# Kernel optimization log

Hardware: AMD Instinct MI355X
Metric: run time of the kernel (lower is better)

The kernel has to match this reference:

```python
import jax, jax.numpy as jnp
import numpy as np

N_NODES = 100000
N_EDGES = 1600000
D_IN = 128
D_OUT = 128


def setup_inputs() -> dict:
    key = jax.random.key(0)
    k1, k2, k3, k4 = jax.random.split(key, 4)
    feat = jax.random.normal(k1, (N_NODES, D_IN), dtype=jnp.float32)
    # xavier_uniform on [D_IN, D_OUT]
    limit = float(np.sqrt(6.0 / (D_IN + D_OUT)))
    weight = jax.random.uniform(k2, (D_IN, D_OUT), minval=-limit, maxval=limit, dtype=jnp.float32)
    bias = jnp.zeros((D_OUT,), dtype=jnp.float32)
    src = jax.random.randint(k3, (N_EDGES,), 0, N_NODES, dtype=jnp.int32)
    dst = jax.random.randint(k4, (N_EDGES,), 0, N_NODES, dtype=jnp.int32)
    return {"feat": feat, "weight": weight, "bias": bias, "src": src, "dst": dst}


def reference(feat, weight, bias, src, dst):
    n = feat.shape[0]
    # in-degree of each node (number of incoming edges)
    deg = jax.ops.segment_sum(jnp.ones_like(dst, dtype=feat.dtype), dst, num_segments=n)
    norm = jnp.power(jnp.clip(deg, 1.0), -0.5)[:, None]  # [N, 1]
    # pre-normalize source features
    h = feat * norm
    # copy_src + sum aggregation: scatter-add messages from src to dst
    agg = jax.ops.segment_sum(h[src], dst, num_segments=n)  # [N, D_IN]
    # in_feats == out_feats -> matmul after aggregation (the else-branch)
    rst = jnp.matmul(agg, weight)
    rst = rst * norm + bias
    return rst
```

## Files before the change

### kernel.cpp

```cpp
#include <hip/hip_runtime.h>

#define D 128
#define BSHIFT 7
#define BNODES 128
#define BMASK 127
#define NB_MAX 1024
#define STRIDE 2944
#define BIN_CHUNK 4096

typedef unsigned int uint;
typedef __attribute__((ext_vector_type(8))) short bf16x8;
typedef __attribute__((ext_vector_type(4))) float f32x4;

__device__ inline uint bf16_rne(float x) {
    uint u = __float_as_uint(x);
    return (u + 0x7fffu + ((u >> 16) & 1u)) >> 16;
}
__device__ inline uint pack2(float lo, float hi) {
    return bf16_rne(lo) | (bf16_rne(hi) << 16);
}

__global__ void __launch_bounds__(256) bin_kernel(const int* __restrict__ src,
                                                  const int* __restrict__ dst,
                                                  int* __restrict__ bucket_cur,
                                                  uint* __restrict__ binned,
                                                  const float* __restrict__ W,
                                                  uint4* __restrict__ wpack,
                                                  int n_edges, int nchunks) {
    int t = threadIdx.x;
    if (blockIdx.x == (uint)nchunks) {
        for (int idx = t; idx < 2048; idx += 256) {
            int lane = idx & 63;
            int ks = (idx >> 6) & 3;
            int ct = idx >> 8;
            int col = ct * 16 + (lane & 15);
            int k0 = ks * 32 + (lane >> 4) * 8;
            uint4 u;
            u.x = pack2(W[(k0 + 0) * D + col], W[(k0 + 1) * D + col]);
            u.y = pack2(W[(k0 + 2) * D + col], W[(k0 + 3) * D + col]);
            u.z = pack2(W[(k0 + 4) * D + col], W[(k0 + 5) * D + col]);
            u.w = pack2(W[(k0 + 6) * D + col], W[(k0 + 7) * D + col]);
            wpack[idx] = u;
        }
        return;
    }

    __shared__ int h[NB_MAX];
    __shared__ int base[NB_MAX];
    long long e0 = (long long)blockIdx.x * BIN_CHUNK;
    for (int j = t; j < NB_MAX; j += 256) h[j] = 0;
    __syncthreads();

    int d[16], s[16];
#pragma unroll
    for (int k = 0; k < 16; ++k) {
        long long idx = e0 + k * 256 + t;
        if (idx < n_edges) {
            d[k] = dst[idx];
            s[k] = src[idx];
            atomicAdd(&h[d[k] >> BSHIFT], 1);
        } else {
            d[k] = -1;
        }
    }
    __syncthreads();
    for (int j = t; j < NB_MAX; j += 256) {
        int c = h[j];
        base[j] = c ? atomicAdd(&bucket_cur[j], c) : 0;
        h[j] = 0;
    }
    __syncthreads();
#pragma unroll
    for (int k = 0; k < 16; ++k) {
        if (d[k] >= 0) {
            int b = d[k] >> BSHIFT;
            int r = base[b] + atomicAdd(&h[b], 1);
            if (r < STRIDE)
                binned[(size_t)b * STRIDE + r] =
                    ((uint)s[k] << BSHIFT) | (uint)(d[k] & BMASK);
        }
    }
}

__global__ void __launch_bounds__(256) fill2_kernel(
        const int* __restrict__ bucket_cur, uint* __restrict__ csr,
        int* __restrict__ row_start, int* __restrict__ degp, int n_nodes) {
    __shared__ uint sbin[STRIDE];
    __shared__ int deg[BNODES];
    __shared__ int rs[BNODES];
    __shared__ int cur[BNODES];
    int b = blockIdx.x;
    int t = threadIdx.x;
    int cnt = bucket_cur[b];
    if (cnt > STRIDE) cnt = STRIDE;
    size_t gbase = (size_t)b * STRIDE;

    for (int k = t; k < cnt; k += 256) sbin[k] = csr[gbase + k];
    if (t < BNODES) deg[t] = 0;
    __syncthreads();
    for (int k = t; k < cnt; k += 256) atomicAdd(&deg[sbin[k] & BMASK], 1);
    __syncthreads();

    int v = 0;
    if (t < BNODES) {
        v = deg[t];
        rs[t] = v;
    }
    __syncthreads();
    for (int o = 1; o < BNODES; o <<= 1) {
        int a = (t < BNODES && t >= o) ? rs[t - o] : 0;
        __syncthreads();
        if (t < BNODES) rs[t] += a;
        __syncthreads();
    }
    if (t < BNODES) {
        int excl = rs[t] - v;
        rs[t] = excl;
        cur[t] = 0;
        int node = b * BNODES + t;
        if (node < n_nodes) {
            row_start[node] = (int)gbase + excl;
            degp[node] = v;
        }
    }
    __syncthreads();

    for (int k = t; k < cnt; k += 256) {
        uint p = sbin[k];
        int dl = p & BMASK;
        int r = atomicAdd(&cur[dl], 1);
        csr[gbase + rs[dl] + r] = p >> BSHIFT;
    }
}

#define GP_ROWS 64
#define GLDP 132
__global__ void __launch_bounds__(256) gemm_prep_kernel(
        const float* __restrict__ feat, const int* __restrict__ degp,
        const uint4* __restrict__ wpack, uint* __restrict__ g32, int n) {
    __shared__ float As[GP_ROWS][GLDP];
    int t = threadIdx.x;
    int lane = t & 63;
    int w = t >> 6;
    int r0 = blockIdx.x * GP_ROWS;

    for (int idx = t; idx < GP_ROWS * 32; idx += 256) {
        int row = idx >> 5;
        int p = idx & 31;
        int gr = r0 + row;
        if (gr >= n) gr = n - 1;
        float4 f = *(const float4*)(feat + (size_t)gr * D + p * 4);
        *(float4*)&As[row][p * 4] = f;
    }
    __syncthreads();

    int c = lane & 15;
    int g = lane >> 4;
    int rbase = w * 16;

    uint4 afr[4];
#pragma unroll
    for (int ks = 0; ks < 4; ++ks) {
        const float* ap = &As[rbase + c][ks * 32 + g * 8];
        float4 f0 = *(const float4*)ap;
        float4 f1 = *(const float4*)(ap + 4);
        afr[ks].x = pack2(f0.x, f0.y);
        afr[ks].y = pack2(f0.z, f0.w);
        afr[ks].z = pack2(f1.x, f1.y);
        afr[ks].w = pack2(f1.z, f1.w);
    }

    float nm[4];
#pragma unroll
    for (int r = 0; r < 4; ++r) {
        int gr = r0 + rbase + g * 4 + r;
        int rc = gr < n ? gr : n - 1;
        nm[r] = rsqrtf(fmaxf((float)degp[rc], 1.0f));
    }

#pragma unroll
    for (int ct = 0; ct < 8; ++ct) {
        f32x4 acc = {0.f, 0.f, 0.f, 0.f};
#pragma unroll
        for (int ks = 0; ks < 4; ++ks) {
            uint4 bu = wpack[(ct * 4 + ks) * 64 + lane];
            acc = __builtin_amdgcn_mfma_f32_16x16x32_bf16(
                *(bf16x8*)&afr[ks], *(bf16x8*)&bu, acc, 0, 0, 0);
        }
#pragma unroll
        for (int r = 0; r < 4; ++r)
            As[rbase + g * 4 + r][ct * 16 + c] = acc[r] * nm[r];
    }

    for (int idx = lane; idx < 16 * 64; idx += 64) {
        int row = idx >> 6;
        int j = idx & 63;
        int gr = r0 + rbase + row;
        if (gr < n) {
            uint vpk = pack2(As[rbase + row][2 * j], As[rbase + row][2 * j + 1]);
            g32[(size_t)gr * 64 + j] = vpk;
        }
    }
}

#define UNPACK_ADD(u)                              \
    acc[0] += __uint_as_float((u).x << 16);        \
    acc[1] += __uint_as_float((u).x & 0xffff0000u);\
    acc[2] += __uint_as_float((u).y << 16);        \
    acc[3] += __uint_as_float((u).y & 0xffff0000u);\
    acc[4] += __uint_as_float((u).z << 16);        \
    acc[5] += __uint_as_float((u).z & 0xffff0000u);\
    acc[6] += __uint_as_float((u).w << 16);        \
    acc[7] += __uint_as_float((u).w & 0xffff0000u);

__global__ void __launch_bounds__(256) gather_out_kernel(
        const uint4* __restrict__ g128, const uint* __restrict__ csr,
        const int* __restrict__ row_start, const int* __restrict__ degp,
        const float* __restrict__ bias, float* __restrict__ out, int n) {
    int lane = threadIdx.x & 63;
    int wid = threadIdx.x >> 6;
    int i = blockIdx.x * 4 + wid;
    if (i >= n) return;
    int g = lane >> 4;
    int c = lane & 15;
    float4 b_lo = *(const float4*)(bias + 8 * c);
    float4 b_hi = *(const float4*)(bias + 8 * c + 4);

    int beg = row_start[i];
    int dv = degp[i];
    int end = beg + dv;
    float acc[8];
#pragma unroll
    for (int j = 0; j < 8; ++j) acc[j] = 0.f;

    for (int base = beg; base < end; base += 64) {
        int nk = end - base;
        if (nk > 64) nk = 64;
        int epre = (base + lane < end) ? (int)csr[base + lane] : 0;
        int k = 0;
        int kfull = nk & ~7;
        for (; k < kfull; k += 8) {
            int s0 = __shfl(epre, k + g, 64);
            int s1 = __shfl(epre, k + 4 + g, 64);
            uint4 u0 = g128[(size_t)s0 * 16 + c];
            uint4 u1 = g128[(size_t)s1 * 16 + c];
            UNPACK_ADD(u0);
            UNPACK_ADD(u1);
        }
        if (k < nk) {
            int e0 = k + g;
            int e1 = k + 4 + g;
            int s0 = __shfl(epre, e0 & 63, 64);
            int s1 = __shfl(epre, e1 & 63, 64);
            uint4 z = {0u, 0u, 0u, 0u};
            uint4 u0 = (e0 < nk) ? g128[(size_t)s0 * 16 + c] : z;
            uint4 u1 = (e1 < nk) ? g128[(size_t)s1 * 16 + c] : z;
            UNPACK_ADD(u0);
            UNPACK_ADD(u1);
        }
    }

#pragma unroll
    for (int j = 0; j < 8; ++j) {
        acc[j] += __shfl_xor(acc[j], 16, 64);
        acc[j] += __shfl_xor(acc[j], 32, 64);
    }
    if (g == 0) {
        float nrm = rsqrtf(fmaxf((float)dv, 1.0f));
        float4 lo, hi;
        lo.x = acc[0] * nrm + b_lo.x;
        lo.y = acc[1] * nrm + b_lo.y;
        lo.z = acc[2] * nrm + b_lo.z;
        lo.w = acc[3] * nrm + b_lo.w;
        hi.x = acc[4] * nrm + b_hi.x;
        hi.y = acc[5] * nrm + b_hi.y;
        hi.z = acc[6] * nrm + b_hi.z;
        hi.w = acc[7] * nrm + b_hi.w;
        float* orow = out + (size_t)i * D + 8 * c;
        *(float4*)orow = lo;
        *(float4*)(orow + 4) = hi;
    }
}

extern "C" void kernel_launch(void* const* d_in, const int* in_sizes, int n_in,
                              void* d_out, int out_size, void* d_ws, size_t ws_size,
                              hipStream_t stream) {
    const float* feat   = (const float*)d_in[0];
    const float* weight = (const float*)d_in[1];
    const float* bias   = (const float*)d_in[2];
    const int*   src    = (const int*)d_in[3];
    const int*   dst    = (const int*)d_in[4];
    float* out = (float*)d_out;

    int n_nodes = in_sizes[0] / D;
    int n_edges = in_sizes[3];
    int nb = (n_nodes + BNODES - 1) >> BSHIFT;
    int nchunks = (n_edges + BIN_CHUNK - 1) / BIN_CHUNK;

    int*   degp       = (int*)d_ws;
    int*   row_start  = degp + n_nodes;
    int*   bucket_cur = row_start + n_nodes;
    uint*  csr        = (uint*)(bucket_cur + NB_MAX);
    uint*  g32        = csr + (size_t)nb * STRIDE;
    uint4* wpack      = (uint4*)(g32 + (size_t)n_nodes * 64);

    hipMemsetAsync(bucket_cur, 0, NB_MAX * sizeof(int), stream);

    bin_kernel<<<nchunks + 1, 256, 0, stream>>>(src, dst, bucket_cur, csr,
                                                weight, wpack, n_edges, nchunks);
    fill2_kernel<<<nb, 256, 0, stream>>>(bucket_cur, csr, row_start, degp,
                                         n_nodes);
    gemm_prep_kernel<<<(n_nodes + GP_ROWS - 1) / GP_ROWS, 256, 0, stream>>>(
        feat, degp, wpack, g32, n_nodes);
    gather_out_kernel<<<(n_nodes + 3) / 4, 256, 0, stream>>>(
        (const uint4*)g32, csr, row_start, degp, bias, out, n_nodes);
}
```

Measured before the change: 139.0 us.

## Overlap edge binning with feature GEMM by deferring source norm to gather

Removes the GEMM's dependency on degrees by applying the source-side norm in the gather, via a per-node norm array computed in fill. Because of that, the binning and feature-transform GEMM run as independent block ranges of one kernel. The memset and the weight packing move into a small init kernel. The gather now loads one extra norm per edge and does an extra multiply per element, in exchange for overlapping the two front-end stages.

```diff
diff --git a/kernel.cpp b/kernel.cpp
--- a/kernel.cpp
+++ b/kernel.cpp
@@ -7,6 +7,8 @@
 #define NB_MAX 1024
 #define STRIDE 2944
 #define BIN_CHUNK 4096
+#define GP_ROWS 64
+#define GLDP 132
 
 typedef unsigned int uint;
 typedef __attribute__((ext_vector_type(8))) short bf16x8;
@@ -20,15 +22,13 @@
     return bf16_rne(lo) | (bf16_rne(hi) << 16);
 }
 
-__global__ void __launch_bounds__(256) bin_kernel(const int* __restrict__ src,
-                                                  const int* __restrict__ dst,
-                                                  int* __restrict__ bucket_cur,
-                                                  uint* __restrict__ binned,
-                                                  const float* __restrict__ W,
-                                                  uint4* __restrict__ wpack,
-                                                  int n_edges, int nchunks) {
+__global__ void __launch_bounds__(256) init_kernel(int* __restrict__ bucket_cur,
+                                                   const float* __restrict__ W,
+                                                   uint4* __restrict__ wpack) {
     int t = threadIdx.x;
-    if (blockIdx.x == (uint)nchunks) {
+    if (blockIdx.x == 0) {
+        for (int j = t; j < NB_MAX; j += 256) bucket_cur[j] = 0;
+    } else {
         for (int idx = t; idx < 2048; idx += 256) {
             int lane = idx & 63;
             int ks = (idx >> 6) & 3;
@@ -42,49 +42,115 @@
             u.w = pack2(W[(k0 + 6) * D + col], W[(k0 + 7) * D + col]);
             wpack[idx] = u;
         }
+    }
+}
+
+__global__ void __launch_bounds__(256) mega_kernel(
+        const int* __restrict__ src, const int* __restrict__ dst,
+        int* __restrict__ bucket_cur, uint* __restrict__ binned,
+        const float* __restrict__ feat, const uint4* __restrict__ wpack,
+        uint* __restrict__ g32, int n_edges, int nchunks, int n) {
+    __shared__ float As[GP_ROWS][GLDP];
+    int t = threadIdx.x;
+
+    if (blockIdx.x < (uint)nchunks) {
+        int* h = (int*)&As[0][0];
+        int* base = h + NB_MAX;
+        long long e0 = (long long)blockIdx.x * BIN_CHUNK;
+        for (int j = t; j < NB_MAX; j += 256) h[j] = 0;
+        __syncthreads();
+
+        int d[16], s[16];
+#pragma unroll
+        for (int k = 0; k < 16; ++k) {
+            long long idx = e0 + k * 256 + t;
+            if (idx < n_edges) {
+                d[k] = dst[idx];
+                s[k] = src[idx];
+                atomicAdd(&h[d[k] >> BSHIFT], 1);
+            } else {
+                d[k] = -1;
+            }
+        }
+        __syncthreads();
+        for (int j = t; j < NB_MAX; j += 256) {
+            int c = h[j];
+            base[j] = c ? atomicAdd(&bucket_cur[j], c) : 0;
+            h[j] = 0;
+        }
+        __syncthreads();
+#pragma unroll
+        for (int k = 0; k < 16; ++k) {
+            if (d[k] >= 0) {
+                int b = d[k] >> BSHIFT;
+                int r = base[b] + atomicAdd(&h[b], 1);
+                if (r < STRIDE)
+                    binned[(size_t)b * STRIDE + r] =
+                        ((uint)s[k] << BSHIFT) | (uint)(d[k] & BMASK);
+            }
+        }
         return;
     }
 
-    __shared__ int h[NB_MAX];
-    __shared__ int base[NB_MAX];
-    long long e0 = (long long)blockIdx.x * BIN_CHUNK;
-    for (int j = t; j < NB_MAX; j += 256) h[j] = 0;
-    __syncthreads();
-
-    int d[16], s[16];
-#pragma unroll
-    for (int k = 0; k < 16; ++k) {
-        long long idx = e0 + k * 256 + t;
-        if (idx < n_edges) {
-            d[k] = dst[idx];
-            s[k] = src[idx];
-            atomicAdd(&h[d[k] >> BSHIFT], 1);
-        } else {
-            d[k] = -1;
-        }
-    }
-    __syncthreads();
-    for (int j = t; j < NB_MAX; j += 256) {
-        int c = h[j];
-        base[j] = c ? atomicAdd(&bucket_cur[j], c) : 0;
-        h[j] = 0;
-    }
-    __syncthreads();
-#pragma unroll
-    for (int k = 0; k < 16; ++k) {
-        if (d[k] >= 0) {
-            int b = d[k] >> BSHIFT;
-            int r = base[b] + atomicAdd(&h[b], 1);
-            if (r < STRIDE)
-                binned[(size_t)b * STRIDE + r] =
-                    ((uint)s[k] << BSHIFT) | (uint)(d[k] & BMASK);
+    int lane = t & 63;
+    int w = t >> 6;
+    int r0 = (blockIdx.x - nchunks) * GP_ROWS;
+
+    for (int idx = t; idx < GP_ROWS * 32; idx += 256) {
+        int row = idx >> 5;
+        int p = idx & 31;
+        int gr = r0 + row;
+        if (gr >= n) gr = n - 1;
+        float4 f = *(const float4*)(feat + (size_t)gr * D + p * 4);
+        *(float4*)&As[row][p * 4] = f;
+    }
+    __syncthreads();
+
+    int c = lane & 15;
+    int g = lane >> 4;
+    int rbase = w * 16;
+
+    uint4 afr[4];
+#pragma unroll
+    for (int ks = 0; ks < 4; ++ks) {
+        const float* ap = &As[rbase + c][ks * 32 + g * 8];
+        float4 f0 = *(const float4*)ap;
+        float4 f1 = *(const float4*)(ap + 4);
+        afr[ks].x = pack2(f0.x, f0.y);
+        afr[ks].y = pack2(f0.z, f0.w);
+        afr[ks].z = pack2(f1.x, f1.y);
+        afr[ks].w = pack2(f1.z, f1.w);
+    }
+
+#pragma unroll
+    for (int ct = 0; ct < 8; ++ct) {
+        f32x4 acc = {0.f, 0.f, 0.f, 0.f};
+#pragma unroll
+        for (int ks = 0; ks < 4; ++ks) {
+            uint4 bu = wpack[(ct * 4 + ks) * 64 + lane];
+            acc = __builtin_amdgcn_mfma_f32_16x16x32_bf16(
+                *(bf16x8*)&afr[ks], *(bf16x8*)&bu, acc, 0, 0, 0);
+        }
+#pragma unroll
+        for (int r = 0; r < 4; ++r)
+            As[rbase + g * 4 + r][ct * 16 + c] = acc[r];
+    }
+
+    for (int idx = lane; idx < 16 * 64; idx += 64) {
+        int row = idx >> 6;
+        int j = idx & 63;
+        int gr = r0 + rbase + row;
+        if (gr < n) {
+            uint vpk = pack2(As[rbase + row][2 * j], As[rbase + row][2 * j + 1]);
+            g32[(size_t)gr * 64 + j] = vpk;
         }
     }
 }
 
 __global__ void __launch_bounds__(256) fill2_kernel(
         const int* __restrict__ bucket_cur, uint* __restrict__ csr,
-        int* __restrict__ row_start, int* __restrict__ degp, int n_nodes) {
+        int* __restrict__ row_start, int* __restrict__ degp,
+        float* __restrict__ norm, int n_nodes) {
     __shared__ uint sbin[STRIDE];
     __shared__ int deg[BNODES];
     __shared__ int rs[BNODES];
@@ -121,6 +187,7 @@
         if (node < n_nodes) {
             row_start[node] = (int)gbase + excl;
             degp[node] = v;
+            norm[node] = rsqrtf(fmaxf((float)v, 1.0f));
         }
     }
     __syncthreads();
@@ -133,90 +200,21 @@
     }
 }
 
-#define GP_ROWS 64
-#define GLDP 132
-__global__ void __launch_bounds__(256) gemm_prep_kernel(
-        const float* __restrict__ feat, const int* __restrict__ degp,
-        const uint4* __restrict__ wpack, uint* __restrict__ g32, int n) {
-    __shared__ float As[GP_ROWS][GLDP];
-    int t = threadIdx.x;
-    int lane = t & 63;
-    int w = t >> 6;
-    int r0 = blockIdx.x * GP_ROWS;
-
-    for (int idx = t; idx < GP_ROWS * 32; idx += 256) {
-        int row = idx >> 5;
-        int p = idx & 31;
-        int gr = r0 + row;
-        if (gr >= n) gr = n - 1;
-        float4 f = *(const float4*)(feat + (size_t)gr * D + p * 4);
-        *(float4*)&As[row][p * 4] = f;
-    }
-    __syncthreads();
-
-    int c = lane & 15;
-    int g = lane >> 4;
-    int rbase = w * 16;
-
-    uint4 afr[4];
-#pragma unroll
-    for (int ks = 0; ks < 4; ++ks) {
-        const float* ap = &As[rbase + c][ks * 32 + g * 8];
-        float4 f0 = *(const float4*)ap;
-        float4 f1 = *(const float4*)(ap + 4);
-        afr[ks].x = pack2(f0.x, f0.y);
-        afr[ks].y = pack2(f0.z, f0.w);
-        afr[ks].z = pack2(f1.x, f1.y);
-        afr[ks].w = pack2(f1.z, f1.w);
-    }
-
-    float nm[4];
-#pragma unroll
-    for (int r = 0; r < 4; ++r) {
-        int gr = r0 + rbase + g * 4 + r;
-        int rc = gr < n ? gr : n - 1;
-        nm[r] = rsqrtf(fmaxf((float)degp[rc], 1.0f));
-    }
-
-#pragma unroll
-    for (int ct = 0; ct < 8; ++ct) {
-        f32x4 acc = {0.f, 0.f, 0.f, 0.f};
-#pragma unroll
-        for (int ks = 0; ks < 4; ++ks) {
-            uint4 bu = wpack[(ct * 4 + ks) * 64 + lane];
-            acc = __builtin_amdgcn_mfma_f32_16x16x32_bf16(
-                *(bf16x8*)&afr[ks], *(bf16x8*)&bu, acc, 0, 0, 0);
-        }
-#pragma unroll
-        for (int r = 0; r < 4; ++r)
-            As[rbase + g * 4 + r][ct * 16 + c] = acc[r] * nm[r];
-    }
-
-    for (int idx = lane; idx < 16 * 64; idx += 64) {
-        int row = idx >> 6;
-        int j = idx & 63;
-        int gr = r0 + rbase + row;
-        if (gr < n) {
-            uint vpk = pack2(As[rbase + row][2 * j], As[rbase + row][2 * j + 1]);
-            g32[(size_t)gr * 64 + j] = vpk;
-        }
-    }
-}
-
-#define UNPACK_ADD(u)                              \
-    acc[0] += __uint_as_float((u).x << 16);        \
-    acc[1] += __uint_as_float((u).x & 0xffff0000u);\
-    acc[2] += __uint_as_float((u).y << 16);        \
-    acc[3] += __uint_as_float((u).y & 0xffff0000u);\
-    acc[4] += __uint_as_float((u).z << 16);        \
-    acc[5] += __uint_as_float((u).z & 0xffff0000u);\
-    acc[6] += __uint_as_float((u).w << 16);        \
-    acc[7] += __uint_as_float((u).w & 0xffff0000u);
+#define UNPACK_FMA(u, nmv)                                   \
+    acc[0] += __uint_as_float((u).x << 16) * (nmv);          \
+    acc[1] += __uint_as_float((u).x & 0xffff0000u) * (nmv);  \
+    acc[2] += __uint_as_float((u).y << 16) * (nmv);          \
+    acc[3] += __uint_as_float((u).y & 0xffff0000u) * (nmv);  \
+    acc[4] += __uint_as_float((u).z << 16) * (nmv);          \
+    acc[5] += __uint_as_float((u).z & 0xffff0000u) * (nmv);  \
+    acc[6] += __uint_as_float((u).w << 16) * (nmv);          \
+    acc[7] += __uint_as_float((u).w & 0xffff0000u) * (nmv);
 
 __global__ void __launch_bounds__(256) gather_out_kernel(
         const uint4* __restrict__ g128, const uint* __restrict__ csr,
         const int* __restrict__ row_start, const int* __restrict__ degp,
-        const float* __restrict__ bias, float* __restrict__ out, int n) {
+        const float* __restrict__ norm, const float* __restrict__ bias,
+        float* __restrict__ out, int n) {
     int lane = threadIdx.x & 63;
     int wid = threadIdx.x >> 6;
     int i = blockIdx.x * 4 + wid;
@@ -237,26 +235,31 @@
         int nk = end - base;
         if (nk > 64) nk = 64;
         int epre = (base + lane < end) ? (int)csr[base + lane] : 0;
+        float npre = norm[epre];
         int k = 0;
         int kfull = nk & ~7;
         for (; k < kfull; k += 8) {
             int s0 = __shfl(epre, k + g, 64);
             int s1 = __shfl(epre, k + 4 + g, 64);
+            float nm0 = __shfl(npre, k + g, 64);
+            float nm1 = __shfl(npre, k + 4 + g, 64);
             uint4 u0 = g128[(size_t)s0 * 16 + c];
             uint4 u1 = g128[(size_t)s1 * 16 + c];
-            UNPACK_ADD(u0);
-            UNPACK_ADD(u1);
+            UNPACK_FMA(u0, nm0);
+            UNPACK_FMA(u1, nm1);
         }
         if (k < nk) {
             int e0 = k + g;
             int e1 = k + 4 + g;
             int s0 = __shfl(epre, e0 & 63, 64);
             int s1 = __shfl(epre, e1 & 63, 64);
+            float nm0 = __shfl(npre, e0 & 63, 64);
+            float nm1 = __shfl(npre, e1 & 63, 64);
             uint4 z = {0u, 0u, 0u, 0u};
             uint4 u0 = (e0 < nk) ? g128[(size_t)s0 * 16 + c] : z;
             uint4 u1 = (e1 < nk) ? g128[(size_t)s1 * 16 + c] : z;
-            UNPACK_ADD(u0);
-            UNPACK_ADD(u1);
+            UNPACK_FMA(u0, nm0);
+            UNPACK_FMA(u1, nm1);
         }
     }
 
@@ -296,22 +299,21 @@
     int n_edges = in_sizes[3];
     int nb = (n_nodes + BNODES - 1) >> BSHIFT;
     int nchunks = (n_edges + BIN_CHUNK - 1) / BIN_CHUNK;
-
-    int*   degp       = (int*)d_ws;
+    int ngemm = (n_nodes + GP_ROWS - 1) / GP_ROWS;
+
+    float* norm       = (float*)d_ws;
+    int*   degp       = (int*)(norm + n_nodes);
     int*   row_start  = degp + n_nodes;
     int*   bucket_cur = row_start + n_nodes;
     uint*  csr        = (uint*)(bucket_cur + NB_MAX);
     uint*  g32        = csr + (size_t)nb * STRIDE;
     uint4* wpack      = (uint4*)(g32 + (size_t)n_nodes * 64);
 
-    hipMemsetAsync(bucket_cur, 0, NB_MAX * sizeof(int), stream);
-
-    bin_kernel<<<nchunks + 1, 256, 0, stream>>>(src, dst, bucket_cur, csr,
-                                                weight, wpack, n_edges, nchunks);
-    fill2_kernel<<<nb, 256, 0, stream>>>(bucket_cur, csr, row_start, degp,
+    init_kernel<<<2, 256, 0, stream>>>(bucket_cur, weight, wpack);
+    mega_kernel<<<nchunks + ngemm, 256, 0, stream>>>(
+        src, dst, bucket_cur, csr, feat, wpack, g32, n_edges, nchunks, n_nodes);
+    fill2_kernel<<<nb, 256, 0, stream>>>(bucket_cur, csr, row_start, degp, norm,
                                          n_nodes);
-    gemm_prep_kernel<<<(n_nodes + GP_ROWS - 1) / GP_ROWS, 256, 0, stream>>>(
-        feat, degp, wpack, g32, n_nodes);
     gather_out_kernel<<<(n_nodes + 3) / 4, 256, 0, stream>>>(
-        (const uint4*)g32, csr, row_start, degp, bias, out, n_nodes);
-}
+        (const uint4*)g32, csr, row_start, degp, norm, bias, out, n_nodes);
+}
```

After: 120.4 us. 13.3% less time.
